# Optimization experiments

Measured on AMD Instinct MI355X. Metric: run time of the kernel, lower is better.

The kernel has to match this reference:

```python
import jax, jax.numpy as jnp
import numpy as np

N_NODES = 50000
N_EDGES = 800000
D_IN = 64
H1 = 64
H2 = 64
N_CLASSES = 10
N_GRAPHS = 500


def setup_inputs() -> dict:
    key = jax.random.key(0)
    ks = jax.random.split(key, 9)
    x = jax.random.normal(ks[0], (N_NODES, D_IN), dtype=jnp.float32)
    edge_index = jax.random.randint(ks[1], (2, N_EDGES), 0, N_NODES, dtype=jnp.int64)
    batch = jnp.sort(jax.random.randint(ks[2], (N_NODES,), 0, N_GRAPHS, dtype=jnp.int64))
    # Linear params (Kaiming-uniform-ish scale)
    def lin(k, fin, fout):
        kw, kb = jax.random.split(k)
        s = 1.0 / np.sqrt(fin)
        W = jax.random.uniform(kw, (fin, fout), minval=-s, maxval=s, dtype=jnp.float32)
        b = jax.random.uniform(kb, (fout,), minval=-s, maxval=s, dtype=jnp.float32)
        return W, b
    W1, b1 = lin(ks[3], D_IN, H1)
    W2, b2 = lin(ks[4], H1, H2)
    W3, b3 = lin(ks[5], H2, N_CLASSES)
    return {"x": x, "edge_index": edge_index, "batch": batch,
            "W1": W1, "b1": b1, "W2": W2, "b2": b2, "W3": W3, "b3": b3}


def _gin_conv(h, src, dst, W, b, eps=0.0):
    # sum aggregation of neighbor messages: msg[i] = sum_{(j->i)} h[j]
    agg = jax.ops.segment_sum(h[src], dst, num_segments=N_NODES)
    return ((1.0 + eps) * h + agg) @ W + b


def reference(x, edge_index, batch, W1, b1, W2, b2, W3, b3):
    src, dst = edge_index[0], edge_index[1]
    h = jax.nn.relu(_gin_conv(x, src, dst, W1, b1))
    h = jax.nn.relu(_gin_conv(h, src, dst, W2, b2))
    # global mean pool over graphs
    sums = jax.ops.segment_sum(h, batch, num_segments=N_GRAPHS)
    cnt = jax.ops.segment_sum(jnp.ones((N_NODES,), dtype=h.dtype), batch, num_segments=N_GRAPHS)
    pooled = sums / jnp.maximum(cnt, 1.0)[:, None]
    return pooled @ W3 + b3
```

## Files before the change

### kernel.cpp

```cpp
#include <hip/hip_runtime.h>
#include <hip/hip_bf16.h>
#include <hip/hip_fp16.h>


#define N_FEAT 64
#define CHUNK 4096
#define CAP 6144

typedef _Float16 f16;
typedef _Float16 half8 __attribute__((ext_vector_type(8)));
typedef float float4v __attribute__((ext_vector_type(4)));

__device__ inline f16 cvt_f16(float v) { return (f16)v; }
__device__ inline f16 cvt_f16(f16 v) { return v; }

template <typename TIN>
__device__ __forceinline__ void gemm_body(const TIN* __restrict__ X, const float* __restrict__ W,
                                          f16* __restrict__ Z, int nrows, int bidx, char* smemc) {
    f16 (*sX)[72] = (f16 (*)[72])smemc;
    f16 (*sWT)[72] = (f16 (*)[72])(smemc + 64 * 72 * sizeof(f16));
    int t = threadIdx.x;
    int base = bidx * 64;
    for (int idx = t; idx < 4096; idx += 256) {
        int k = idx >> 6, n = idx & 63;
        sWT[n][k] = (f16)W[idx];
    }
    for (int idx = t; idx < 4096; idx += 256) {
        int r = idx >> 6, c = idx & 63;
        int row = base + r;
        sX[r][c] = (row < nrows) ? cvt_f16(X[(size_t)row * 64 + c]) : (f16)0.f;
    }
    __syncthreads();
    int wave = t >> 6;
    int lane = t & 63;
    int quad = lane >> 4;
    int m16 = lane & 15;
    half8 a0 = *(const half8*)&sX[wave * 16 + m16][quad * 8];
    half8 a1 = *(const half8*)&sX[wave * 16 + m16][32 + quad * 8];
    float4v acc[4];
#pragma unroll
    for (int C = 0; C < 4; ++C) {
        half8 b0 = *(const half8*)&sWT[C * 16 + m16][quad * 8];
        half8 b1 = *(const half8*)&sWT[C * 16 + m16][32 + quad * 8];
        float4v d = {0.f, 0.f, 0.f, 0.f};
        d = __builtin_amdgcn_mfma_f32_16x16x32_f16(a0, b0, d, 0, 0, 0);
        d = __builtin_amdgcn_mfma_f32_16x16x32_f16(a1, b1, d, 0, 0, 0);
        acc[C] = d;
    }
#pragma unroll
    for (int reg = 0; reg < 4; ++reg) {
        int row = base + wave * 16 + quad * 4 + reg;
        if (row < nrows) {
#pragma unroll
            for (int C = 0; C < 4; ++C)
                Z[(size_t)row * 64 + C * 16 + m16] = (f16)acc[C][reg];
        }
    }
}

template <typename TIN>
__global__ __launch_bounds__(256) void gemm_mfma(const TIN* __restrict__ X, const float* __restrict__ W,
                                                 f16* __restrict__ Z, int nrows) {
    __shared__ __align__(16) char smem[2 * 64 * 72 * sizeof(f16)];
    gemm_body<TIN>(X, W, Z, nrows, blockIdx.x, smem);
}

__global__ __launch_bounds__(256) void bucket_scatter(const int* __restrict__ src, const int* __restrict__ dst,
                               int* __restrict__ ccur, int* __restrict__ staging, int E) {
    __shared__ int epack[CHUNK];
    __shared__ int ebkt[CHUNK];
    __shared__ int hist[256];
    __shared__ int base[256];
    int t = threadIdx.x;
    int begin = blockIdx.x * CHUNK;
    int cnt = min(CHUNK, E - begin);
    hist[t] = 0;
    __syncthreads();
    for (int i = t; i < cnt; i += 256) {
        int d = dst[begin + i];
        int s = src[begin + i];
        epack[i] = (s & 0xFFFF) | ((d & 255) << 16);
        ebkt[i] = d >> 8;
        atomicAdd(&hist[d >> 8], 1);
    }
    __syncthreads();
    int h = hist[t];
    if (h > 0) base[t] = atomicAdd(&ccur[t], h);
    hist[t] = 0;
    __syncthreads();
    for (int i = t; i < cnt; i += 256) {
        int b = ebkt[i];
        int off = base[b] + atomicAdd(&hist[b], 1);
        if (off < CAP) staging[(size_t)b * CAP + off] = epack[i];
    }
}

__device__ __forceinline__ void finalize_body(const int* __restrict__ staging, const int* __restrict__ ccur,
                                              int2* __restrict__ rowse, int* __restrict__ col, int N,
                                              int b, char* smemc) {
    int* edges = (int*)smemc;
    int* hist = edges + CAP;
    int* scan = hist + 256;
    int* cur = scan + 256;
    int t = threadIdx.x;
    int cnt = min(ccur[b], CAP);
    int sbase = b * CAP;
    hist[t] = 0;
    __syncthreads();
    for (int i = t; i < cnt; i += 256) {
        int e = staging[(size_t)sbase + i];
        edges[i] = e;
        atomicAdd(&hist[(e >> 16) & 255], 1);
    }
    __syncthreads();
    int v = hist[t];
    scan[t] = v;
    __syncthreads();
    for (int off = 1; off < 256; off <<= 1) {
        int u = (t >= off) ? scan[t - off] : 0;
        __syncthreads();
        scan[t] += u;
        __syncthreads();
    }
    int excl = scan[t] - v;
    cur[t] = excl;
    int node = b * 256 + t;
    if (node < N) rowse[node] = make_int2(sbase + excl, sbase + excl + v);
    __syncthreads();
    for (int i = t; i < cnt; i += 256) {
        int e = edges[i];
        int pos = sbase + atomicAdd(&cur[(e >> 16) & 255], 1);
        col[pos] = e & 0xFFFF;
    }
}

__global__ __launch_bounds__(256) void fused_finalize_gemm(
        const int* __restrict__ staging, const int* __restrict__ ccur,
        int2* __restrict__ rowse, int* __restrict__ col, int N,
        const float* __restrict__ X, const float* __restrict__ W,
        f16* __restrict__ Z, int nrows, int nbf) {
    __shared__ __align__(16) char smem[(CAP + 768) * 4];
    if ((int)blockIdx.x < nbf)
        finalize_body(staging, ccur, rowse, col, N, blockIdx.x, smem);
    else
        gemm_body<float>(X, W, Z, nrows, blockIdx.x - nbf, smem);
}

template <int POOL>
__global__ __launch_bounds__(256) void gather_relu2(
        const f16* __restrict__ Z, const int2* __restrict__ rowse,
        const int* __restrict__ col, const float* __restrict__ bias,
        f16* __restrict__ H, float* __restrict__ sums,
        const int* __restrict__ batch, int n) {
    __shared__ float sh[4][64];
    __shared__ int gid[4];
    int w = threadIdx.x >> 6;
    int node = (int)(blockIdx.x * 4 + w);
    int lane = threadIdx.x & 63;
    int e = lane >> 3, c = lane & 7;
    bool valid = node < n;
    int lo = 0, hi = 0;
    if (valid) { int2 se = rowse[node]; lo = se.x; hi = se.y; }
    const float4v* Z4 = reinterpret_cast<const float4v*>(Z);
    float acc[8] = {0.f, 0.f, 0.f, 0.f, 0.f, 0.f, 0.f, 0.f};
    int idx[4];
#pragma unroll
    for (int i = 0; i < 4; ++i) {
        int j = lo + e + i * 8;
        idx[i] = (j < hi) ? col[j] : -1;
    }
#pragma unroll
    for (int i = 0; i < 4; ++i) {
        if (idx[i] >= 0) {
            float4v r = Z4[(size_t)idx[i] * 8 + c];
            half8 hv = *(half8*)&r;
#pragma unroll
            for (int k = 0; k < 8; ++k) acc[k] += (float)hv[k];
        }
    }
    for (int j = lo + 32 + e; j < hi; j += 8) {
        float4v r = Z4[(size_t)col[j] * 8 + c];
        half8 hv = *(half8*)&r;
#pragma unroll
        for (int k = 0; k < 8; ++k) acc[k] += (float)hv[k];
    }
#pragma unroll
    for (int k = 0; k < 8; ++k) {
        acc[k] += __shfl_xor(acc[k], 8);
        acc[k] += __shfl_xor(acc[k], 16);
        acc[k] += __shfl_xor(acc[k], 32);
    }
    if (POOL) {
        if (lane == 0) gid[w] = valid ? batch[node] : -1;
    }
    if (valid && e == 0) {
        float4v sr = Z4[(size_t)node * 8 + c];
        half8 sv = *(half8*)&sr;
        const float4* B4 = reinterpret_cast<const float4*>(bias);
        float4 b0 = B4[c * 2];
        float4 b1 = B4[c * 2 + 1];
        float bb[8] = {b0.x, b0.y, b0.z, b0.w, b1.x, b1.y, b1.z, b1.w};
        float h[8];
#pragma unroll
        for (int k = 0; k < 8; ++k) h[k] = fmaxf((float)sv[k] + acc[k] + bb[k], 0.f);
        if (!POOL) {
            half8 o;
#pragma unroll
            for (int k = 0; k < 8; ++k) o[k] = (f16)h[k];
            reinterpret_cast<half8*>(H)[(size_t)node * 8 + c] = o;
        } else {
#pragma unroll
            for (int k = 0; k < 8; ++k) sh[w][c * 8 + k] = h[k];
        }
    }
    if (POOL) {
        __syncthreads();
        if (w == 0) {
            int cg = gid[0];
            float run = 0.f;
#pragma unroll
            for (int q = 0; q < 4; ++q) {
                int g = gid[q];
                if (g < 0) break;
                if (g != cg) {
                    atomicAdd(&sums[cg * 64 + lane], run);
                    run = 0.f;
                    cg = g;
                }
                run += sh[q][lane];
            }
            if (cg >= 0) atomicAdd(&sums[cg * 64 + lane], run);
        }
    }
}

__global__ __launch_bounds__(64) void head_kernel(
        const float* __restrict__ sums, const int* __restrict__ batch,
        const float* __restrict__ W3, const float* __restrict__ b3,
        float* __restrict__ out, int n, int ncls) {
    int g = blockIdx.x;
    __shared__ float row[64];
    __shared__ int bnd[2];
    int t = threadIdx.x;
    if (t < 2) {
        int target = g + t;
        int lo = 0, hi = n;
        while (lo < hi) { int m = (lo + hi) >> 1; if (batch[m] < target) lo = m + 1; else hi = m; }
        bnd[t] = lo;
    }
    __syncthreads();
    float cnt = fmaxf((float)(bnd[1] - bnd[0]), 1.0f);
    row[t] = sums[g * 64 + t] / cnt;
    __syncthreads();
    if (t < ncls) {
        float o = b3[t];
#pragma unroll
        for (int k = 0; k < 64; ++k) o += row[k] * W3[k * ncls + t];
        out[g * ncls + t] = o;
    }
}

extern "C" void kernel_launch(void* const* d_in, const int* in_sizes, int n_in,
                              void* d_out, int out_size, void* d_ws, size_t ws_size,
                              hipStream_t stream) {
    const float* x     = (const float*)d_in[0];
    const int*   ei    = (const int*)d_in[1];
    const int*   batch = (const int*)d_in[2];
    const float* W1    = (const float*)d_in[3];
    const float* b1    = (const float*)d_in[4];
    const float* W2    = (const float*)d_in[5];
    const float* b2    = (const float*)d_in[6];
    const float* W3    = (const float*)d_in[7];
    const float* b3    = (const float*)d_in[8];
    float* out = (float*)d_out;

    const int N = in_sizes[0] / N_FEAT;
    const int E = in_sizes[1] / 2;
    const int NCLS = 10;
    const int G = out_size / NCLS;
    const int* src = ei;
    const int* dst = ei + E;
    const int nb = (N + 255) / 256;

    int*   staging = (int*)d_ws;
    int2*  rowse   = (int2*)(staging + (size_t)nb * CAP);
    int*   col     = (int*)(rowse + N);
    int*   ccur    = col + (size_t)nb * CAP;
    float* sums    = (float*)(ccur + 256);
    f16*   zbuf    = (f16*)(sums + (size_t)G * 64);
    f16*   hbuf    = zbuf + (size_t)N * 64;

    const int gemmGrid = (N + 63) / 64;
    const int gatherGrid = (N + 3) / 4;
    const int scatGrid = (E + CHUNK - 1) / CHUNK;

    hipMemsetAsync(ccur, 0, (256 + (size_t)G * 64) * sizeof(int), stream);
    bucket_scatter<<<scatGrid, 256, 0, stream>>>(src, dst, ccur, staging, E);

    fused_finalize_gemm<<<nb + gemmGrid, 256, 0, stream>>>(
        staging, ccur, rowse, col, N, x, W1, zbuf, N, nb);

    gather_relu2<0><<<gatherGrid, 256, 0, stream>>>(zbuf, rowse, col, b1, hbuf, nullptr, nullptr, N);

    gemm_mfma<f16><<<gemmGrid, 256, 0, stream>>>(hbuf, W2, zbuf, N);
    gather_relu2<1><<<gatherGrid, 256, 0, stream>>>(zbuf, rowse, col, b2, nullptr, sums, batch, N);

    head_kernel<<<G, 64, 0, stream>>>(sums, batch, W3, b3, out, N, NCLS);
}
```

Before: 176.7 us.

## Fuse layer-1 gather/ReLU with layer-2 GEMM into one kernel

Replaces the separate first-layer gather kernel and the second GEMM kernel with one gather_gemm kernel. Each 512-thread block aggregates neighbours for 32 nodes, applies bias and ReLU into shared memory, then multiplies by W2 with MFMA and writes Z2 directly. This drops a kernel launch and the round trip of the intermediate H buffer through global memory. In exchange every block reconverts W2 into shared memory, and each block covers fewer rows, which may affect occupancy.

```diff
diff --git a/kernel.cpp b/kernel.cpp
--- a/kernel.cpp
+++ b/kernel.cpp
@@ -56,13 +56,6 @@
                 Z[(size_t)row * 64 + C * 16 + m16] = (f16)acc[C][reg];
         }
     }
-}
-
-template <typename TIN>
-__global__ __launch_bounds__(256) void gemm_mfma(const TIN* __restrict__ X, const float* __restrict__ W,
-                                                 f16* __restrict__ Z, int nrows) {
-    __shared__ __align__(16) char smem[2 * 64 * 72 * sizeof(f16)];
-    gemm_body<TIN>(X, W, Z, nrows, blockIdx.x, smem);
 }
 
 __global__ __launch_bounds__(256) void bucket_scatter(const int* __restrict__ src, const int* __restrict__ dst,
@@ -144,6 +137,95 @@
         finalize_body(staging, ccur, rowse, col, N, blockIdx.x, smem);
     else
         gemm_body<float>(X, W, Z, nrows, blockIdx.x - nbf, smem);
+}
+
+__global__ __launch_bounds__(512) void gather_gemm(
+        const f16* __restrict__ Z, const int2* __restrict__ rowse,
+        const int* __restrict__ col, const float* __restrict__ bias,
+        const float* __restrict__ W2, f16* __restrict__ Z2, int n) {
+    __shared__ f16 sH[32][72];
+    __shared__ f16 sWT[64][72];
+    int t = threadIdx.x;
+    for (int idx = t; idx < 4096; idx += 512) {
+        int k = idx >> 6, nn = idx & 63;
+        sWT[nn][k] = (f16)W2[idx];
+    }
+    int w = t >> 6;
+    int lane = t & 63;
+    int e = lane >> 3, c = lane & 7;
+    int base = blockIdx.x * 32;
+    const float4v* Z4 = reinterpret_cast<const float4v*>(Z);
+    const float4* B4 = reinterpret_cast<const float4*>(bias);
+#pragma unroll
+    for (int q = 0; q < 4; ++q) {
+        int node = base + w * 4 + q;
+        bool valid = node < n;
+        int lo = 0, hi = 0;
+        if (valid) { int2 se = rowse[node]; lo = se.x; hi = se.y; }
+        float acc[8] = {0.f, 0.f, 0.f, 0.f, 0.f, 0.f, 0.f, 0.f};
+        int idx4[4];
+#pragma unroll
+        for (int i = 0; i < 4; ++i) {
+            int j = lo + e + i * 8;
+            idx4[i] = (j < hi) ? col[j] : -1;
+        }
+#pragma unroll
+        for (int i = 0; i < 4; ++i) {
+            if (idx4[i] >= 0) {
+                float4v r = Z4[(size_t)idx4[i] * 8 + c];
+                half8 hv = *(half8*)&r;
+#pragma unroll
+                for (int k = 0; k < 8; ++k) acc[k] += (float)hv[k];
+            }
+        }
+        for (int j = lo + 32 + e; j < hi; j += 8) {
+            float4v r = Z4[(size_t)col[j] * 8 + c];
+            half8 hv = *(half8*)&r;
+#pragma unroll
+            for (int k = 0; k < 8; ++k) acc[k] += (float)hv[k];
+        }
+#pragma unroll
+        for (int k = 0; k < 8; ++k) {
+            acc[k] += __shfl_xor(acc[k], 8);
+            acc[k] += __shfl_xor(acc[k], 16);
+            acc[k] += __shfl_xor(acc[k], 32);
+        }
+        if (e == 0) {
+            half8 o;
+            if (valid) {
+                float4v sr = Z4[(size_t)node * 8 + c];
+                half8 sv = *(half8*)&sr;
+                float4 b0 = B4[c * 2];
+                float4 b1 = B4[c * 2 + 1];
+                float bb[8] = {b0.x, b0.y, b0.z, b0.w, b1.x, b1.y, b1.z, b1.w};
+#pragma unroll
+                for (int k = 0; k < 8; ++k)
+                    o[k] = (f16)fmaxf((float)sv[k] + acc[k] + bb[k], 0.f);
+            } else {
+#pragma unroll
+                for (int k = 0; k < 8; ++k) o[k] = (f16)0.f;
+            }
+            *(half8*)&sH[w * 4 + q][c * 8] = o;
+        }
+    }
+    __syncthreads();
+    int quad = lane >> 4;
+    int m16 = lane & 15;
+    int mrow = (w >> 2) * 16;
+    int ncol = (w & 3) * 16;
+    half8 a0 = *(const half8*)&sH[mrow + m16][quad * 8];
+    half8 a1 = *(const half8*)&sH[mrow + m16][32 + quad * 8];
+    half8 b0 = *(const half8*)&sWT[ncol + m16][quad * 8];
+    half8 b1 = *(const half8*)&sWT[ncol + m16][32 + quad * 8];
+    float4v d = {0.f, 0.f, 0.f, 0.f};
+    d = __builtin_amdgcn_mfma_f32_16x16x32_f16(a0, b0, d, 0, 0, 0);
+    d = __builtin_amdgcn_mfma_f32_16x16x32_f16(a1, b1, d, 0, 0, 0);
+#pragma unroll
+    for (int reg = 0; reg < 4; ++reg) {
+        int row = base + mrow + quad * 4 + reg;
+        if (row < n)
+            Z2[(size_t)row * 64 + ncol + m16] = (f16)d[reg];
+    }
 }
 
 template <int POOL>
@@ -288,9 +370,10 @@
     int*   ccur    = col + (size_t)nb * CAP;
     float* sums    = (float*)(ccur + 256);
     f16*   zbuf    = (f16*)(sums + (size_t)G * 64);
-    f16*   hbuf    = zbuf + (size_t)N * 64;
+    f16*   z2buf   = zbuf + (size_t)N * 64;
 
     const int gemmGrid = (N + 63) / 64;
+    const int gg2Grid  = (N + 31) / 32;
     const int gatherGrid = (N + 3) / 4;
     const int scatGrid = (E + CHUNK - 1) / CHUNK;
 
@@ -300,10 +383,9 @@
     fused_finalize_gemm<<<nb + gemmGrid, 256, 0, stream>>>(
         staging, ccur, rowse, col, N, x, W1, zbuf, N, nb);
 
-    gather_relu2<0><<<gatherGrid, 256, 0, stream>>>(zbuf, rowse, col, b1, hbuf, nullptr, nullptr, N);
-
-    gemm_mfma<f16><<<gemmGrid, 256, 0, stream>>>(hbuf, W2, zbuf, N);
-    gather_relu2<1><<<gatherGrid, 256, 0, stream>>>(zbuf, rowse, col, b2, nullptr, sums, batch, N);
+    gather_gemm<<<gg2Grid, 512, 0, stream>>>(zbuf, rowse, col, b1, W2, z2buf, N);
+
+    gather_relu2<1><<<gatherGrid, 256, 0, stream>>>(z2buf, rowse, col, b2, nullptr, sums, batch, N);
 
     head_kernel<<<G, 64, 0, stream>>>(sums, batch, W3, b3, out, N, NCLS);
 }
```

Measured after the change: 169.4 us. 4.1% less time.
